# Optimization experiments

Measured on AMD Instinct MI355X. Metric: run time of the kernel, lower is better.

## Reference

```python
import jax, jax.numpy as jnp
import numpy as np

B, G, S, L, F = 2, 1024, 64, 16, 8   # batch, attention windows, tokens/window, cells/token, in_features
ATT, RANK, HC = 128, 32, 32          # att_dim, factorization rank, n_head_channels
LF = L * F


def setup_inputs() -> dict:
    key = jax.random.key(0)
    ks = jax.random.split(key, 14)
    s = 0.05
    return {
        "x": jax.random.normal(ks[0], (B, G, S, L, F), jnp.float32),
        # rank-factorized Q projection: (L*F) -> att_dim
        "Wq_u": jax.random.normal(ks[1], (LF, RANK), jnp.float32) * s,
        "Wq_v": jax.random.normal(ks[2], (RANK, ATT), jnp.float32) * s,
        # rank-factorized KV projection: (L*F) -> 2*att_dim (bias=True in source)
        "Wkv_u": jax.random.normal(ks[3], (LF, RANK), jnp.float32) * s,
        "Wkv_v": jax.random.normal(ks[4], (RANK, 2 * ATT), jnp.float32) * s,
        "kv_b": jnp.zeros((2 * ATT,), jnp.float32),
        # rank-factorized out layer: att_dim -> (L*F)
        "Wo_u": jax.random.normal(ks[5], (ATT, RANK), jnp.float32) * s,
        "Wo_v": jax.random.normal(ks[6], (RANK, LF), jnp.float32) * s,
        # per-token-element residual gate (init 1e-7 as in source)
        "gamma": jnp.full((L, F), 1e-7, jnp.float32),
        # factorized MLP: (L*F) -> att_dim -> (L*F)
        "W1": jax.random.normal(ks[7], (LF, ATT), jnp.float32) * s,
        "b1": jnp.zeros((ATT,), jnp.float32),
        "W2": jax.random.normal(ks[8], (ATT, LF), jnp.float32) * s,
        "b2": jnp.zeros((LF,), jnp.float32),
        "gamma_mlp": jnp.full((), 1e-7, jnp.float32),
    }


def _ln(t):
    # layer norm over the token dims (L, F), no affine
    m = t.mean(axis=(-2, -1), keepdims=True)
    v = t.var(axis=(-2, -1), keepdims=True)
    return (t - m) * jax.lax.rsqrt(v + 1e-5)


def reference(x, Wq_u, Wq_v, Wkv_u, Wkv_v, kv_b, Wo_u, Wo_v, gamma, W1, b1, W2, b2, gamma_mlp):
    b, g, sfx, l, f = x.shape
    lf = l * f
    h = _ln(x).reshape(b, g, sfx, lf)                 # [b,g,s,LF]
    q = (h @ Wq_u) @ Wq_v                              # [b,g,s,ATT]
    kv = (h @ Wkv_u) @ Wkv_v + kv_b                    # [b,g,s,2*ATT]
    k, v = jnp.split(kv, 2, axis=-1)
    nh = q.shape[-1] // HC
    def heads(t):
        return t.reshape(b, g, sfx, nh, HC).transpose(0, 1, 3, 2, 4)  # [b,g,H,s,hc]
    qh, kh, vh = heads(q), heads(k), heads(v)
    scores = jnp.einsum('bghsc,bghtc->bghst', qh, kh) / np.float32(np.sqrt(HC))
    attn = jax.nn.softmax(scores, axis=-1)             # [b,g,H,s,s]
    o = jnp.einsum('bghst,bghtc->bghsc', attn, vh)
    o = o.transpose(0, 1, 3, 2, 4).reshape(b, g, sfx, nh * HC)
    upd = ((o @ Wo_u) @ Wo_v).reshape(b, g, sfx, l, f)
    x1 = x + gamma * upd                               # 'shift' update with gamma gate
    h2 = _ln(x1).reshape(b, g, sfx, lf)
    m = jax.nn.gelu(h2 @ W1 + b1) @ W2 + b2
    return x1 + gamma_mlp * m.reshape(b, g, sfx, l, f)
```

## Files before the change

kernel.cpp:

```cpp
#include <hip/hip_runtime.h>

#define NWIN 2048

#define WUT8_OFF 0
#define MT8_OFF  8192
#define OT8_OFF  12288
#define W1T_OFF  28672
#define W2T8_OFF 61440
#define CVEC_OFF 77824

typedef __attribute__((ext_vector_type(8))) __bf16 bf16x8;
typedef __attribute__((ext_vector_type(8))) short s16x8;
typedef __attribute__((ext_vector_type(4))) short s16x4;
typedef __attribute__((ext_vector_type(4))) float f32x4;

static __device__ inline short f2bf(float f) {
    __bf16 b = (__bf16)f;
    return __builtin_bit_cast(short, b);
}
static __device__ inline float bf2f(short h) {
    unsigned u = ((unsigned)(unsigned short)h) << 16;
    return __builtin_bit_cast(float, u);
}
static __device__ inline bf16x8 ldbf8(const short* p) {
    return __builtin_bit_cast(bf16x8, *(const s16x8*)p);
}
static __device__ inline unsigned char f2fp8(float v) {
    return (unsigned char)__builtin_amdgcn_cvt_pk_fp8_f32(v, v, 0u, false);
}
static __device__ inline long ld8(const void* p) {
    return *(const long*)p;
}

__global__ __launch_bounds__(256) void fam_pre(
    const float* __restrict__ Wq_u, const float* __restrict__ Wq_v,
    const float* __restrict__ Wkv_u, const float* __restrict__ Wkv_v,
    const float* __restrict__ kv_b, const float* __restrict__ Wo_u,
    const float* __restrict__ Wo_v, const float* __restrict__ W1,
    const float* __restrict__ W2, unsigned char* __restrict__ ws8)
{
    const int b = blockIdx.x, tid = threadIdx.x;
    float* cvec = (float*)(ws8 + CVEC_OFF);
    if (b < 16) {
        __shared__ float Wv[4096];
        __shared__ float Wu[4096];
        __shared__ float N[4096];
        for (int i = tid; i < 4096; i += 256) {
            int r = i >> 7, c = i & 127;
            Wv[i] = Wkv_v[r*256 + 128 + c];
            Wu[i] = Wo_u[i];
        }
        __syncthreads();
        for (int i = tid; i < 4096; i += 256) {
            int h = i >> 10, u = (i >> 5) & 31, r = i & 31;
            float acc = 0.f;
            for (int c = 0; c < 32; ++c) acc += Wv[r*128 + h*32 + c] * Wu[(h*32 + c)*32 + u];
            N[i] = acc;
        }
        __syncthreads();
        for (int i = tid; i < 1024; i += 256) {
            int jj = i >> 7, hr = i & 127;
            int j = b*8 + jj, h = hr >> 5, r = hr & 31;
            float acc = 0.f;
            for (int u = 0; u < 32; ++u) acc += N[h*1024 + u*32 + r] * Wo_v[u*128 + j];
            ws8[OT8_OFF + j*128 + hr] = f2fp8(acc * 128.f);
        }
    } else if (b < 32) {
        short* w1t = (short*)(ws8 + W1T_OFF);
        int i0 = (b - 16) * 8;
        for (int t = tid; t < 1024; t += 256) {
            int ii = t >> 7, k = t & 127, i = i0 + ii;
            w1t[i*128 + k] = f2bf(W1[k*128 + i]);
        }
    } else if (b < 48) {
        int j0 = (b - 32) * 8;
        for (int t = tid; t < 1024; t += 256) {
            int jj = t >> 7, k = t & 127, j = j0 + jj;
            ws8[W2T8_OFF + j*128 + k] = f2fp8(W2[k*128 + j] * 16.f);
        }
    } else {
        __shared__ float Aq[4096];
        __shared__ float Ak[4096];
        __shared__ float ov[32];
        for (int i = tid; i < 4096; i += 256) {
            int r = i >> 7, c = i & 127;
            Aq[i] = Wq_v[i];
            Ak[i] = Wkv_v[r*256 + c];
        }
        for (int i = tid; i < 8192; i += 256) {
            int n = i >> 7, k = i & 127;
            float w = (n < 32) ? Wq_u[k*32 + n] : Wkv_u[k*32 + (n - 32)];
            ws8[WUT8_OFF + n*128 + k] = f2fp8(w * 16.f);
        }
        __syncthreads();
        const float sc = 0.17677669529663687f * 256.f;
        for (int i = tid; i < 4096; i += 256) {
            int h = i >> 10, r = (i >> 5) & 31, u = i & 31;
            float acc = 0.f;
            for (int c = 0; c < 32; ++c) acc += Aq[u*128 + h*32 + c] * Ak[r*128 + h*32 + c];
            ws8[MT8_OFF + h*1024 + r*32 + u] = f2fp8(acc * sc);
        }
        if (tid < 32) {
            float a = 0.f;
            for (int att = 0; att < 128; ++att) a += kv_b[128 + att] * Wo_u[att*32 + tid];
            ov[tid] = a;
        }
        __syncthreads();
        if (tid < 128) {
            float a = 0.f;
            for (int u = 0; u < 32; ++u) a += ov[u] * Wo_v[u*128 + tid];
            cvec[tid] = a;
        }
    }
}

#define SRA 136
#define SHQ 40
#define SHB 72

#define SM_RA8   0
#define SM_HUQ8  8704
#define SM_KV8   11264
#define SM_KVT8  13824
#define SM_HB8   16128
#define SM_TOTAL 34560

__global__ __launch_bounds__(256, 4) void fam_main(
    const float* __restrict__ x, const unsigned char* __restrict__ ws8,
    const float* __restrict__ gamma, const float* __restrict__ b1,
    const float* __restrict__ b2, const float* __restrict__ gmlp_p,
    float* __restrict__ out)
{
    __shared__ __align__(16) unsigned char SM[SM_TOTAL];
    unsigned char* RA8  = SM + SM_RA8;
    unsigned char* HUQ8 = SM + SM_HUQ8;
    unsigned char* KV8  = SM + SM_KV8;
    unsigned char* KVT8 = SM + SM_KVT8;

    const float* cvec = (const float*)(ws8 + CVEC_OFF);
    const int tid = threadIdx.x;
    const int l   = tid & 63;
    const int wv  = tid >> 6;
    const int l15 = l & 15;
    const int lg  = l >> 4;
    const size_t base = (size_t)blockIdx.x * 8192;
    const float* __restrict__ xw   = x + base;
    float* __restrict__       outw = out + base;
    const int n0 = wv * 32;

    {
        int s = tid >> 2, c = tid & 3;
        float4 xr1[8];
        float sum = 0.f, sq = 0.f;
        #pragma unroll
        for (int j = 0; j < 8; ++j) {
            xr1[j] = *(const float4*)&xw[s*128 + c*32 + j*4];
            sum += xr1[j].x + xr1[j].y + xr1[j].z + xr1[j].w;
            sq  += xr1[j].x*xr1[j].x + xr1[j].y*xr1[j].y + xr1[j].z*xr1[j].z + xr1[j].w*xr1[j].w;
        }
        sum += __shfl_xor(sum, 1); sq += __shfl_xor(sq, 1);
        sum += __shfl_xor(sum, 2); sq += __shfl_xor(sq, 2);
        float mean = sum * (1.f/128.f);
        float var  = sq * (1.f/128.f) - mean*mean;
        float rinv = rsqrtf(var + 1e-5f);
        #pragma unroll
        for (int j = 0; j < 8; ++j) {
            unsigned w = 0;
            w = __builtin_amdgcn_cvt_pk_fp8_f32((xr1[j].x - mean)*rinv, (xr1[j].y - mean)*rinv, w, false);
            w = __builtin_amdgcn_cvt_pk_fp8_f32((xr1[j].z - mean)*rinv, (xr1[j].w - mean)*rinv, w, true);
            *(unsigned*)&RA8[s*SRA + c*32 + j*4] = w;
        }
    }
    __syncthreads();

    {
        long bfr[4];
        #pragma unroll
        for (int kb = 0; kb < 4; ++kb)
            bfr[kb] = ld8(ws8 + WUT8_OFF + (wv*16 + l15)*128 + kb*32 + lg*8);
        #pragma unroll
        for (int m = 0; m < 4; ++m) {
            f32x4 acc = {0.f, 0.f, 0.f, 0.f};
            #pragma unroll
            for (int kb = 0; kb < 4; ++kb) {
                long a = ld8(RA8 + (m*16 + l15)*SRA + kb*32 + lg*8);
                acc = __builtin_amdgcn_mfma_f32_16x16x32_fp8_fp8(a, bfr[kb], acc, 0, 0, 0);
            }
            if (wv < 2) {
                int col = wv*16 + l15;
                #pragma unroll
                for (int j = 0; j < 4; ++j)
                    HUQ8[(m*16 + lg*4 + j)*SHQ + col] = f2fp8(acc[j] * 0.25f);
            } else {
                int u = (wv - 2)*16 + l15;
                #pragma unroll
                for (int j = 0; j < 4; ++j)
                    KV8[(m*16 + lg*4 + j)*SHQ + u] = f2fp8(acc[j] * 0.25f);
                unsigned w = 0;
                w = __builtin_amdgcn_cvt_pk_fp8_f32(acc[0]*0.25f, acc[1]*0.25f, w, false);
                w = __builtin_amdgcn_cvt_pk_fp8_f32(acc[2]*0.25f, acc[3]*0.25f, w, true);
                *(unsigned*)&KVT8[u*SHB + m*16 + lg*4] = w;
            }
        }
    }
    __syncthreads();

    {
        const int h = wv;
        unsigned char* HB8h = SM + SM_HB8 + h*4608;
        long bm0 = ld8(ws8 + MT8_OFF + h*1024 + l15*32 + lg*8);
        long bm1 = ld8(ws8 + MT8_OFF + h*1024 + (16 + l15)*32 + lg*8);
        #pragma unroll
        for (int m = 0; m < 4; ++m) {
            long aq = ld8(HUQ8 + (m*16 + l15)*SHQ + lg*8);
            f32x4 z = {0.f, 0.f, 0.f, 0.f};
            f32x4 a0 = __builtin_amdgcn_mfma_f32_16x16x32_fp8_fp8(aq, bm0, z, 0, 0, 0);
            f32x4 a1 = __builtin_amdgcn_mfma_f32_16x16x32_fp8_fp8(aq, bm1, z, 0, 0, 0);
            #pragma unroll
            for (int j = 0; j < 4; ++j) {
                int row = (m*16 + lg*4 + j)*SHB;
                HB8h[row + l15]      = f2fp8(a0[j] * 0.0625f);
                HB8h[row + 16 + l15] = f2fp8(a1[j] * 0.0625f);
            }
        }
        long av[4], bq[4];
        #pragma unroll
        for (int m = 0; m < 4; ++m) av[m] = ld8(KV8 + (m*16 + l15)*SHQ + lg*8);
        #pragma unroll
        for (int n = 0; n < 4; ++n) bq[n] = ld8(HB8h + (n*16 + l15)*SHB + lg*8);
        f32x4 cc[4][4];
        #pragma unroll
        for (int m = 0; m < 4; ++m)
            #pragma unroll
            for (int n = 0; n < 4; ++n) {
                f32x4 z = {0.f, 0.f, 0.f, 0.f};
                cc[m][n] = __builtin_amdgcn_mfma_f32_16x16x32_fp8_fp8(av[m], bq[n], z, 0, 0, 0);
            }
        #pragma unroll
        for (int n = 0; n < 4; ++n) {
            float e[4][4];
            float sm = 0.f;
            #pragma unroll
            for (int m = 0; m < 4; ++m)
                #pragma unroll
                for (int j = 0; j < 4; ++j) {
                    e[m][j] = __expf(fminf(cc[m][n][j] * 0.00390625f, 30.f));
                    sm += e[m][j];
                }
            sm += __shfl_xor(sm, 16);
            sm += __shfl_xor(sm, 32);
            float rs64 = __builtin_amdgcn_rcpf(sm) * 64.f;
            int srow = (n*16 + l15) * SHB;
            #pragma unroll
            for (int m = 0; m < 4; ++m) {
                unsigned w = 0;
                w = __builtin_amdgcn_cvt_pk_fp8_f32(e[m][0]*rs64, e[m][1]*rs64, w, false);
                w = __builtin_amdgcn_cvt_pk_fp8_f32(e[m][2]*rs64, e[m][3]*rs64, w, true);
                *(unsigned*)&HB8h[srow + m*16 + lg*4] = w;
            }
        }
        long a8[4][2], b8[2][2];
        #pragma unroll
        for (int m = 0; m < 4; ++m)
            #pragma unroll
            for (int kb = 0; kb < 2; ++kb)
                a8[m][kb] = ld8(HB8h + (m*16 + l15)*SHB + kb*32 + lg*8);
        #pragma unroll
        for (int nn = 0; nn < 2; ++nn)
            #pragma unroll
            for (int kb = 0; kb < 2; ++kb)
                b8[nn][kb] = ld8(KVT8 + (nn*16 + l15)*SHB + kb*32 + lg*8);
        #pragma unroll
        for (int m = 0; m < 4; ++m)
            #pragma unroll
            for (int nn = 0; nn < 2; ++nn) {
                f32x4 acc = {0.f,0.f,0.f,0.f};
                acc = __builtin_amdgcn_mfma_f32_16x16x32_fp8_fp8(a8[m][0], b8[nn][0], acc, 0, 0, 0);
                acc = __builtin_amdgcn_mfma_f32_16x16x32_fp8_fp8(a8[m][1], b8[nn][1], acc, 0, 0, 0);
                #pragma unroll
                for (int j = 0; j < 4; ++j)
                    RA8[(m*16 + lg*4 + j)*SRA + h*32 + nn*16 + l15] = f2fp8(acc[j] * 0.03125f);
            }
    }
    __syncthreads();

    float x1v[4][2][4];
    short* XB = (short*)(SM + SM_HB8);

    {
        float xr[4][2][4];
        #pragma unroll
        for (int m = 0; m < 4; ++m)
            #pragma unroll
            for (int nn = 0; nn < 2; ++nn)
                #pragma unroll
                for (int j = 0; j < 4; ++j)
                    xr[m][nn][j] = xw[(m*16 + lg*4 + j)*128 + n0 + nn*16 + l15];
        long bo[2][4];
        float cv[2], gm[2];
        #pragma unroll
        for (int nn = 0; nn < 2; ++nn) {
            int col = n0 + nn*16 + l15;
            #pragma unroll
            for (int kb = 0; kb < 4; ++kb)
                bo[nn][kb] = ld8(ws8 + OT8_OFF + col*128 + kb*32 + lg*8);
            cv[nn] = cvec[col];
            gm[nn] = gamma[col];
        }
        f32x4 acc[4][2];
        #pragma unroll
        for (int m = 0; m < 4; ++m)
            #pragma unroll
            for (int nn = 0; nn < 2; ++nn) acc[m][nn] = (f32x4){0.f,0.f,0.f,0.f};
        #pragma unroll
        for (int m = 0; m < 4; ++m) {
            long a[4];
            #pragma unroll
            for (int kb = 0; kb < 4; ++kb)
                a[kb] = ld8(RA8 + (m*16 + l15)*SRA + kb*32 + lg*8);
            #pragma unroll
            for (int kb = 0; kb < 4; ++kb)
                #pragma unroll
                for (int nn = 0; nn < 2; ++nn)
                    acc[m][nn] = __builtin_amdgcn_mfma_f32_16x16x32_fp8_fp8(a[kb], bo[nn][kb], acc[m][nn], 0, 0, 0);
        }
        #pragma unroll
        for (int m = 0; m < 4; ++m)
            #pragma unroll
            for (int nn = 0; nn < 2; ++nn)
                #pragma unroll
                for (int j = 0; j < 4; ++j) {
                    int row = m*16 + lg*4 + j;
                    float v = xr[m][nn][j] + gm[nn] * (acc[m][nn][j] * 9.765625e-4f + cv[nn]);
                    x1v[m][nn][j] = v;
                    XB[row*SRA + n0 + nn*16 + l15] = f2bf(v);
                }
    }
    __syncthreads();

    {
        int s = tid >> 2, c = tid & 3;
        float sum = 0.f, sq = 0.f;
        #pragma unroll
        for (int jj = 0; jj < 8; ++jj) {
            s16x4 hv = *(const s16x4*)&XB[s*SRA + c*32 + jj*4];
            #pragma unroll
            for (int e = 0; e < 4; ++e) {
                float f = bf2f(hv[e]);
                sum += f; sq += f*f;
            }
        }
        sum += __shfl_xor(sum, 1); sq += __shfl_xor(sq, 1);
        sum += __shfl_xor(sum, 2); sq += __shfl_xor(sq, 2);
        float mean = sum * (1.f/128.f);
        float var  = sq * (1.f/128.f) - mean*mean;
        float rinv = rsqrtf(var + 1e-5f);
        #pragma unroll
        for (int jj = 0; jj < 8; ++jj) {
            s16x4 hv = *(const s16x4*)&XB[s*SRA + c*32 + jj*4];
            s16x4 ov;
            #pragma unroll
            for (int e = 0; e < 4; ++e) ov[e] = f2bf((bf2f(hv[e]) - mean) * rinv);
            *(s16x4*)&XB[s*SRA + c*32 + jj*4] = ov;
        }
    }
    __syncthreads();

    {
        const short* W1t = (const short*)(ws8 + W1T_OFF);
        bf16x8 bw1[2][4];
        float bb1[2];
        #pragma unroll
        for (int nn = 0; nn < 2; ++nn) {
            #pragma unroll
            for (int k = 0; k < 4; ++k)
                bw1[nn][k] = ldbf8(&W1t[(n0 + nn*16 + l15)*128 + k*32 + lg*8]);
            bb1[nn] = b1[n0 + nn*16 + l15];
        }
        #pragma unroll
        for (int m = 0; m < 4; ++m) {
            bf16x8 a[4];
            #pragma unroll
            for (int k = 0; k < 4; ++k)
                a[k] = ldbf8(&XB[(m*16 + l15)*SRA + k*32 + lg*8]);
            #pragma unroll
            for (int nn = 0; nn < 2; ++nn) {
                f32x4 acc = {0.f,0.f,0.f,0.f};
                #pragma unroll
                for (int k = 0; k < 4; ++k)
                    acc = __builtin_amdgcn_mfma_f32_16x16x32_bf16(a[k], bw1[nn][k], acc, 0, 0, 0);
                #pragma unroll
                for (int j = 0; j < 4; ++j) {
                    float t = acc[j] + bb1[nn];
                    float w = -1.5957691216057308f * (t + 0.044715f*t*t*t);
                    float g = t * __builtin_amdgcn_rcpf(1.f + __expf(w));
                    RA8[(m*16 + lg*4 + j)*SRA + n0 + nn*16 + l15] = f2fp8(g * 8.f);
                }
            }
        }
    }
    __syncthreads();

    {
        const float gmv = gmlp_p[0];
        long bw[2][4];
        float bb[2];
        #pragma unroll
        for (int nn = 0; nn < 2; ++nn) {
            int col = n0 + nn*16 + l15;
            #pragma unroll
            for (int kb = 0; kb < 4; ++kb)
                bw[nn][kb] = ld8(ws8 + W2T8_OFF + col*128 + kb*32 + lg*8);
            bb[nn] = b2[col];
        }
        #pragma unroll
        for (int m = 0; m < 4; ++m) {
            long a[4];
            #pragma unroll
            for (int kb = 0; kb < 4; ++kb)
                a[kb] = ld8(RA8 + (m*16 + l15)*SRA + kb*32 + lg*8);
            #pragma unroll
            for (int nn = 0; nn < 2; ++nn) {
                f32x4 acc = {0.f,0.f,0.f,0.f};
                #pragma unroll
                for (int kb = 0; kb < 4; ++kb)
                    acc = __builtin_amdgcn_mfma_f32_16x16x32_fp8_fp8(a[kb], bw[nn][kb], acc, 0, 0, 0);
                #pragma unroll
                for (int j = 0; j < 4; ++j)
                    outw[(m*16 + lg*4 + j)*128 + n0 + nn*16 + l15] =
                        x1v[m][nn][j] + gmv * (acc[j] * 0.0078125f + bb[nn]);
            }
        }
    }
}

extern "C" void kernel_launch(void* const* d_in, const int* in_sizes, int n_in,
                              void* d_out, int out_size, void* d_ws, size_t ws_size,
                              hipStream_t stream) {
    const float* x     = (const float*)d_in[0];
    const float* Wq_u  = (const float*)d_in[1];
    const float* Wq_v  = (const float*)d_in[2];
    const float* Wkv_u = (const float*)d_in[3];
    const float* Wkv_v = (const float*)d_in[4];
    const float* kv_b  = (const float*)d_in[5];
    const float* Wo_u  = (const float*)d_in[6];
    const float* Wo_v  = (const float*)d_in[7];
    const float* gamma = (const float*)d_in[8];
    const float* W1    = (const float*)d_in[9];
    const float* b1    = (const float*)d_in[10];
    const float* W2    = (const float*)d_in[11];
    const float* b2    = (const float*)d_in[12];
    const float* gmlp  = (const float*)d_in[13];
    unsigned char* ws8 = (unsigned char*)d_ws;
    float* out = (float*)d_out;

    fam_pre<<<49, 256, 0, stream>>>(Wq_u, Wq_v, Wkv_u, Wkv_v, kv_b, Wo_u, Wo_v, W1, W2, ws8);
    fam_main<<<NWIN, 256, 0, stream>>>(x, ws8, gamma, b1, b2, gmlp, out);
}
```

Before: 89.98 us.

## Fold Q-side score matrix into the Q projection weights in precompute

The per-head score matrix M_h (Wq_v·Wkv_v^T, scaled) is now folded into Wq_u during the weight precompute. This yields a 128x128 combined projection, and each window goes straight from normalized x to per-head query-side factors in one MFMA stage. That removes the intermediate HUQ buffer, one barrier-separated MFMA stage and its fp8 requantization. It adds more MFMAs in the first projection, since each wave now does two or three accumulators per row block. The lower shared-memory footprint lets launch bounds rise to 5 blocks per CU, and the precompute kernel is split across 8 blocks, which changes fp8 rounding.

```diff
diff --git a/kernel.cpp b/kernel.cpp
--- a/kernel.cpp
+++ b/kernel.cpp
@@ -2,12 +2,11 @@
 
 #define NWIN 2048
 
-#define WUT8_OFF 0
-#define MT8_OFF  8192
-#define OT8_OFF  12288
-#define W1T_OFF  28672
-#define W2T8_OFF 61440
-#define CVEC_OFF 77824
+#define QKVT8_OFF 0
+#define OT8_OFF  20480
+#define W1T_OFF  36864
+#define W2T8_OFF 69632
+#define CVEC_OFF 86016
 
 typedef __attribute__((ext_vector_type(8))) __bf16 bf16x8;
 typedef __attribute__((ext_vector_type(8))) short s16x8;
@@ -79,37 +78,41 @@
             ws8[W2T8_OFF + j*128 + k] = f2fp8(W2[k*128 + j] * 16.f);
         }
     } else {
-        __shared__ float Aq[4096];
-        __shared__ float Ak[4096];
+        const int sl = b - 48;
+        __shared__ float Msh[4096];
         __shared__ float ov[32];
+        const float sc = 0.17677669529663687f;
         for (int i = tid; i < 4096; i += 256) {
-            int r = i >> 7, c = i & 127;
-            Aq[i] = Wq_v[i];
-            Ak[i] = Wkv_v[r*256 + c];
-        }
-        for (int i = tid; i < 8192; i += 256) {
-            int n = i >> 7, k = i & 127;
-            float w = (n < 32) ? Wq_u[k*32 + n] : Wkv_u[k*32 + (n - 32)];
-            ws8[WUT8_OFF + n*128 + k] = f2fp8(w * 16.f);
+            int h = i >> 10, u = (i >> 5) & 31, r = i & 31;
+            float acc = 0.f;
+            for (int c = 0; c < 32; ++c)
+                acc += Wq_v[u*128 + h*32 + c] * Wkv_v[r*256 + h*32 + c];
+            Msh[i] = acc * sc;
         }
         __syncthreads();
-        const float sc = 0.17677669529663687f * 256.f;
-        for (int i = tid; i < 4096; i += 256) {
-            int h = i >> 10, r = (i >> 5) & 31, u = i & 31;
+        for (int i = tid; i < 2048; i += 256) {
+            int c = sl*16 + (i >> 7), k = i & 127;
+            int h = c >> 5, r = c & 31;
             float acc = 0.f;
-            for (int c = 0; c < 32; ++c) acc += Aq[u*128 + h*32 + c] * Ak[r*128 + h*32 + c];
-            ws8[MT8_OFF + h*1024 + r*32 + u] = f2fp8(acc * sc);
-        }
-        if (tid < 32) {
-            float a = 0.f;
-            for (int att = 0; att < 128; ++att) a += kv_b[128 + att] * Wo_u[att*32 + tid];
-            ov[tid] = a;
-        }
-        __syncthreads();
-        if (tid < 128) {
-            float a = 0.f;
-            for (int u = 0; u < 32; ++u) a += ov[u] * Wo_v[u*128 + tid];
-            cvec[tid] = a;
+            for (int u = 0; u < 32; ++u) acc += Wq_u[k*32 + u] * Msh[h*1024 + u*32 + r];
+            ws8[QKVT8_OFF + c*128 + k] = f2fp8(acc * 256.f);
+        }
+        for (int i = tid; i < 512; i += 256) {
+            int u = sl*4 + (i >> 7), k = i & 127;
+            ws8[QKVT8_OFF + (128 + u)*128 + k] = f2fp8(Wkv_u[k*32 + u] * 16.f);
+        }
+        if (sl == 0) {
+            if (tid < 32) {
+                float a = 0.f;
+                for (int att = 0; att < 128; ++att) a += kv_b[128 + att] * Wo_u[att*32 + tid];
+                ov[tid] = a;
+            }
+            __syncthreads();
+            if (tid < 128) {
+                float a = 0.f;
+                for (int u = 0; u < 32; ++u) a += ov[u] * Wo_v[u*128 + tid];
+                cvec[tid] = a;
+            }
         }
     }
 }
@@ -119,13 +122,12 @@
 #define SHB 72
 
 #define SM_RA8   0
-#define SM_HUQ8  8704
-#define SM_KV8   11264
-#define SM_KVT8  13824
-#define SM_HB8   16128
-#define SM_TOTAL 34560
-
-__global__ __launch_bounds__(256, 4) void fam_main(
+#define SM_KV8   8704
+#define SM_KVT8  11264
+#define SM_HB8   13568
+#define SM_TOTAL 32000
+
+__global__ __launch_bounds__(256, 5) void fam_main(
     const float* __restrict__ x, const unsigned char* __restrict__ ws8,
     const float* __restrict__ gamma, const float* __restrict__ b1,
     const float* __restrict__ b2, const float* __restrict__ gmlp_p,
@@ -133,7 +135,6 @@
 {
     __shared__ __align__(16) unsigned char SM[SM_TOTAL];
     unsigned char* RA8  = SM + SM_RA8;
-    unsigned char* HUQ8 = SM + SM_HUQ8;
     unsigned char* KV8  = SM + SM_KV8;
     unsigned char* KVT8 = SM + SM_KVT8;
 
@@ -174,31 +175,50 @@
     __syncthreads();
 
     {
-        long bfr[4];
-        #pragma unroll
-        for (int kb = 0; kb < 4; ++kb)
-            bfr[kb] = ld8(ws8 + WUT8_OFF + (wv*16 + l15)*128 + kb*32 + lg*8);
+        long bA[4], bB[4], bC[4];
+        #pragma unroll
+        for (int kb = 0; kb < 4; ++kb) {
+            bA[kb] = ld8(ws8 + QKVT8_OFF + (wv*16 + l15)*128 + kb*32 + lg*8);
+            bB[kb] = ld8(ws8 + QKVT8_OFF + ((wv + 4)*16 + l15)*128 + kb*32 + lg*8);
+        }
+        if (wv >= 2) {
+            #pragma unroll
+            for (int kb = 0; kb < 4; ++kb)
+                bC[kb] = ld8(ws8 + QKVT8_OFF + ((6 + wv)*16 + l15)*128 + kb*32 + lg*8);
+        }
+        unsigned char* HBA = SM + SM_HB8 + (wv >> 1)*4608;
+        unsigned char* HBB = SM + SM_HB8 + (2 + (wv >> 1))*4608;
+        const int rr = (wv & 1)*16 + l15;
         #pragma unroll
         for (int m = 0; m < 4; ++m) {
-            f32x4 acc = {0.f, 0.f, 0.f, 0.f};
+            long a[4];
+            #pragma unroll
+            for (int kb = 0; kb < 4; ++kb)
+                a[kb] = ld8(RA8 + (m*16 + l15)*SRA + kb*32 + lg*8);
+            f32x4 accA = {0.f,0.f,0.f,0.f}, accB = {0.f,0.f,0.f,0.f};
             #pragma unroll
             for (int kb = 0; kb < 4; ++kb) {
-                long a = ld8(RA8 + (m*16 + l15)*SRA + kb*32 + lg*8);
-                acc = __builtin_amdgcn_mfma_f32_16x16x32_fp8_fp8(a, bfr[kb], acc, 0, 0, 0);
-            }
-            if (wv < 2) {
-                int col = wv*16 + l15;
+                accA = __builtin_amdgcn_mfma_f32_16x16x32_fp8_fp8(a[kb], bA[kb], accA, 0, 0, 0);
+                accB = __builtin_amdgcn_mfma_f32_16x16x32_fp8_fp8(a[kb], bB[kb], accB, 0, 0, 0);
+            }
+            #pragma unroll
+            for (int j = 0; j < 4; ++j) {
+                int row = (m*16 + lg*4 + j)*SHB;
+                HBA[row + rr] = f2fp8(accA[j] * 0.25f);
+                HBB[row + rr] = f2fp8(accB[j] * 0.25f);
+            }
+            if (wv >= 2) {
+                f32x4 accC = {0.f,0.f,0.f,0.f};
+                #pragma unroll
+                for (int kb = 0; kb < 4; ++kb)
+                    accC = __builtin_amdgcn_mfma_f32_16x16x32_fp8_fp8(a[kb], bC[kb], accC, 0, 0, 0);
+                int u = (wv - 2)*16 + l15;
                 #pragma unroll
                 for (int j = 0; j < 4; ++j)
-                    HUQ8[(m*16 + lg*4 + j)*SHQ + col] = f2fp8(acc[j] * 0.25f);
-            } else {
-                int u = (wv - 2)*16 + l15;
-                #pragma unroll
-                for (int j = 0; j < 4; ++j)
-                    KV8[(m*16 + lg*4 + j)*SHQ + u] = f2fp8(acc[j] * 0.25f);
+                    KV8[(m*16 + lg*4 + j)*SHQ + u] = f2fp8(accC[j] * 0.25f);
                 unsigned w = 0;
-                w = __builtin_amdgcn_cvt_pk_fp8_f32(acc[0]*0.25f, acc[1]*0.25f, w, false);
-                w = __builtin_amdgcn_cvt_pk_fp8_f32(acc[2]*0.25f, acc[3]*0.25f, w, true);
+                w = __builtin_amdgcn_cvt_pk_fp8_f32(accC[0]*0.25f, accC[1]*0.25f, w, false);
+                w = __builtin_amdgcn_cvt_pk_fp8_f32(accC[2]*0.25f, accC[3]*0.25f, w, true);
                 *(unsigned*)&KVT8[u*SHB + m*16 + lg*4] = w;
             }
         }
@@ -208,21 +228,6 @@
     {
         const int h = wv;
         unsigned char* HB8h = SM + SM_HB8 + h*4608;
-        long bm0 = ld8(ws8 + MT8_OFF + h*1024 + l15*32 + lg*8);
-        long bm1 = ld8(ws8 + MT8_OFF + h*1024 + (16 + l15)*32 + lg*8);
-        #pragma unroll
-        for (int m = 0; m < 4; ++m) {
-            long aq = ld8(HUQ8 + (m*16 + l15)*SHQ + lg*8);
-            f32x4 z = {0.f, 0.f, 0.f, 0.f};
-            f32x4 a0 = __builtin_amdgcn_mfma_f32_16x16x32_fp8_fp8(aq, bm0, z, 0, 0, 0);
-            f32x4 a1 = __builtin_amdgcn_mfma_f32_16x16x32_fp8_fp8(aq, bm1, z, 0, 0, 0);
-            #pragma unroll
-            for (int j = 0; j < 4; ++j) {
-                int row = (m*16 + lg*4 + j)*SHB;
-                HB8h[row + l15]      = f2fp8(a0[j] * 0.0625f);
-                HB8h[row + 16 + l15] = f2fp8(a1[j] * 0.0625f);
-            }
-        }
         long av[4], bq[4];
         #pragma unroll
         for (int m = 0; m < 4; ++m) av[m] = ld8(KV8 + (m*16 + l15)*SHQ + lg*8);
@@ -454,6 +459,6 @@
     unsigned char* ws8 = (unsigned char*)d_ws;
     float* out = (float*)d_out;
 
-    fam_pre<<<49, 256, 0, stream>>>(Wq_u, Wq_v, Wkv_u, Wkv_v, kv_b, Wo_u, Wo_v, W1, W2, ws8);
+    fam_pre<<<56, 256, 0, stream>>>(Wq_u, Wq_v, Wkv_u, Wkv_v, kv_b, Wo_u, Wo_v, W1, W2, ws8);
     fam_main<<<NWIN, 256, 0, stream>>>(x, ws8, gamma, b1, b2, gmlp, out);
 }
```

New measurement: 93.31 us. +3.7%, slower.
